# Kernel tuning notes

Measured on AMD Instinct MI355X. Metric: run time of the kernel, lower is better.

Reference implementation:

```python
import jax, jax.numpy as jnp
import numpy as np

EMBED = 512
HEADS = 8                      # num_heads
HD = EMBED // HEADS // 2       # diff-attn head dim = 32
EXP = 4
DEPTH = 1
LAMBDA_INIT = 0.8 - 0.6 * float(np.exp(-0.3 * (DEPTH - 1)))  # 0.2
EPS = 1e-5


def layernorm(x, w, b):
    mu = jnp.mean(x, axis=-1, keepdims=True)
    var = jnp.mean(jnp.square(x - mu), axis=-1, keepdims=True)
    return (x - mu) * jax.lax.rsqrt(var + EPS) * w + b


def rmsnorm(x, w):
    ms = jnp.mean(jnp.square(x), axis=-1, keepdims=True)
    return x * jax.lax.rsqrt(ms + EPS) * w


def setup_inputs() -> dict:
    key = jax.random.key(0)
    ks = jax.random.split(key, 12)
    B, N, D = 8, 1024, EMBED
    s = 0.02
    inp = {
        "x": jax.random.normal(ks[0], (B, N, D), jnp.float32),
        # diff-attention params
        "Wq": jax.random.normal(ks[1], (D, D), jnp.float32) * s,
        "Wk": jax.random.normal(ks[2], (D, D), jnp.float32) * s,
        "Wv": jax.random.normal(ks[3], (D, D), jnp.float32) * s,
        "Wo": jax.random.normal(ks[4], (D, D), jnp.float32) * s,
        "lq1": jax.random.normal(ks[5], (HD,), jnp.float32) * 0.1,
        "lk1": jax.random.normal(ks[6], (HD,), jnp.float32) * 0.1,
        "lq2": jax.random.normal(ks[7], (HD,), jnp.float32) * 0.1,
        "lk2": jax.random.normal(ks[8], (HD,), jnp.float32) * 0.1,
        "subln_w": jnp.ones((2 * HD,), jnp.float32),
        # block norms
        "n1_w": jnp.ones((D,), jnp.float32), "n1_b": jnp.zeros((D,), jnp.float32),
        "n2_w": jnp.ones((D,), jnp.float32), "n2_b": jnp.zeros((D,), jnp.float32),
        # MLP: LN(D) -> Linear(D,4D) -> GELU -> LN(4D) -> Linear(4D,D)
        "mln1_w": jnp.ones((D,), jnp.float32), "mln1_b": jnp.zeros((D,), jnp.float32),
        "mW1": jax.random.normal(ks[9], (EXP * D, D), jnp.float32) * s,
        "mb1": jnp.zeros((EXP * D,), jnp.float32),
        "mln2_w": jnp.ones((EXP * D,), jnp.float32), "mln2_b": jnp.zeros((EXP * D,), jnp.float32),
        "mW2": jax.random.normal(ks[10], (D, EXP * D), jnp.float32) * s,
        "mb2": jnp.zeros((D,), jnp.float32),
    }
    return inp


def diff_attn(x, Wq, Wk, Wv, Wo, lq1, lk1, lq2, lk2, subln_w):
    B, N, D = x.shape
    q = (x @ Wq.T).reshape(B, N, 2 * HEADS, HD).transpose(0, 2, 1, 3)   # [B,2H,N,hd]
    k = (x @ Wk.T).reshape(B, N, 2 * HEADS, HD).transpose(0, 2, 1, 3)   # [B,2H,N,hd]
    v = (x @ Wv.T).reshape(B, N, HEADS, 2 * HD).transpose(0, 2, 1, 3)   # [B,H,N,2hd]
    q = q * (HD ** -0.5)
    scores = jnp.einsum("bhnd,bhmd->bhnm", q, k)                        # [B,2H,N,N]
    attn = jax.nn.softmax(scores, axis=-1)
    attn = attn.reshape(B, HEADS, 2, N, N)
    lam1 = jnp.exp(jnp.sum(lq1 * lk1))
    lam2 = jnp.exp(jnp.sum(lq2 * lk2))
    lam = lam1 - lam2 + LAMBDA_INIT
    attn = attn[:, :, 0] - lam * attn[:, :, 1]                          # [B,H,N,N]
    out = jnp.einsum("bhnm,bhmd->bhnd", attn, v)                        # [B,H,N,2hd]
    out = rmsnorm(out, subln_w) * (1.0 - LAMBDA_INIT)
    out = out.transpose(0, 2, 1, 3).reshape(B, N, D)
    return out @ Wo.T


def reference(x, Wq, Wk, Wv, Wo, lq1, lk1, lq2, lk2, subln_w,
              n1_w, n1_b, n2_w, n2_b,
              mln1_w, mln1_b, mW1, mb1, mln2_w, mln2_b, mW2, mb2):
    x_res = x
    xn = layernorm(x, n1_w, n1_b)
    a = diff_attn(xn, Wq, Wk, Wv, Wo, lq1, lk1, lq2, lk2, subln_w)
    h = layernorm(a, n2_w, n2_b) + x_res
    # MLP
    z = layernorm(h, mln1_w, mln1_b)
    z = jax.nn.gelu(z @ mW1.T + mb1, approximate=False)
    z = layernorm(z, mln2_w, mln2_b)
    z = z @ mW2.T + mb2
    return z + h
```

## Files before the change

kernel.cpp:

```cpp
#include <hip/hip_runtime.h>
#include <cstdint>
#include <cstddef>

typedef unsigned short u16;
typedef unsigned int   u32;
typedef __attribute__((ext_vector_type(8))) short short8;
typedef __attribute__((ext_vector_type(4))) float floatx4;

__device__ __forceinline__ float asf(u32 u){ union{u32 u; float f;} v; v.u=u; return v.f; }
__device__ __forceinline__ u32 asu(float f){ union{float f; u32 u;} v; v.f=f; return v.u; }
__device__ __forceinline__ u16 f2bf(float f){ u32 u = asu(f); u32 r = u + 0x7FFFu + ((u>>16)&1u); return (u16)(r>>16); }
__device__ __forceinline__ u32 pack2(float a, float b){ return (u32)f2bf(a) | (((u32)f2bf(b))<<16); }
__device__ __forceinline__ void bf8f(uint4 d, float* o){
  o[0]=asf(d.x<<16); o[1]=asf(d.x&0xFFFF0000u);
  o[2]=asf(d.y<<16); o[3]=asf(d.y&0xFFFF0000u);
  o[4]=asf(d.z<<16); o[5]=asf(d.z&0xFFFF0000u);
  o[6]=asf(d.w<<16); o[7]=asf(d.w&0xFFFF0000u);
}

__global__ __launch_bounds__(256) void cvt_all(
    const float* __restrict__ Wq, const float* __restrict__ Wk,
    const float* __restrict__ Wv, const float* __restrict__ Wo,
    const float* __restrict__ W1, const float* __restrict__ W2,
    u16* __restrict__ Wqkv, u16* __restrict__ Wob,
    u16* __restrict__ W1b, u16* __restrict__ W2b)
{
  const int blk = blockIdx.x;
  const float* src; u16* dst; int off;
  if      (blk < 128)  { src = Wq; dst = Wqkv;          off = blk; }
  else if (blk < 256)  { src = Wk; dst = Wqkv + 262144; off = blk - 128; }
  else if (blk < 384)  { src = Wv; dst = Wqkv + 524288; off = blk - 256; }
  else if (blk < 512)  { src = Wo; dst = Wob;           off = blk - 384; }
  else if (blk < 1024) { src = W1; dst = W1b;           off = blk - 512; }
  else                 { src = W2; dst = W2b;           off = blk - 1024; }
  const int i = (off*256 + threadIdx.x)*8;
  const float4 a = *(const float4*)(src + i);
  const float4 b = *(const float4*)(src + i + 4);
  uint4 st;
  st.x = pack2(a.x, a.y); st.y = pack2(a.z, a.w);
  st.z = pack2(b.x, b.y); st.w = pack2(b.z, b.w);
  *(uint4*)(dst + i) = st;
}

enum { EPI_NONE=0, EPI_BIAS_GELU=1, EPI_BIAS_RES=2 };

template<int EPI, typename OutT>
__global__ __launch_bounds__(256) void gemm_bt(
    const u16* __restrict__ A, const u16* __restrict__ B,
    const float* __restrict__ bias, const float* __restrict__ res,
    OutT* __restrict__ C, int M, int N, int K)
{
  __shared__ u16 As[128*32];
  __shared__ u16 Bs[128*32];
  const int tid  = threadIdx.x;
  const int wave = tid >> 6;
  const int lane = tid & 63;
  const int bm = blockIdx.y, bn = blockIdx.x;

  const int srow = wave*16 + (lane>>2);
  const int scol = (lane&3)*8;
  const u16* Ag = A + (size_t)bm*128*K;
  const u16* Bg = B + (size_t)bn*128*K;

  const int wm = (wave>>1)*64;
  const int wn = (wave&1)*64;
  const int fr = lane & 15;
  const int fk = (lane>>4)*8;

  floatx4 acc[4][4] = {};

  for (int k0 = 0; k0 < K; k0 += 32) {
    __syncthreads();
    #pragma unroll
    for (int t = 0; t < 2; ++t) {
      __builtin_amdgcn_global_load_lds(
          (__attribute__((address_space(1))) void*)(Ag + (t*64 + srow)*K + k0 + scol),
          (__attribute__((address_space(3))) void*)(As + (t*64 + wave*16)*32),
          16, 0, 0);
      __builtin_amdgcn_global_load_lds(
          (__attribute__((address_space(1))) void*)(Bg + (t*64 + srow)*K + k0 + scol),
          (__attribute__((address_space(3))) void*)(Bs + (t*64 + wave*16)*32),
          16, 0, 0);
    }
    __syncthreads();

    short8 af[4], bfr[4];
    #pragma unroll
    for (int i=0;i<4;i++) af[i]  = *(const short8*)(As + (wm + i*16 + fr)*32 + fk);
    #pragma unroll
    for (int j=0;j<4;j++) bfr[j] = *(const short8*)(Bs + (wn + j*16 + fr)*32 + fk);
    #pragma unroll
    for (int i=0;i<4;i++)
      #pragma unroll
      for (int j=0;j<4;j++)
        acc[i][j] = __builtin_amdgcn_mfma_f32_16x16x32_bf16(af[i], bfr[j], acc[i][j], 0, 0, 0);
  }

  const int col0 = bn*128 + wn + fr;
  float bv[4] = {0.f,0.f,0.f,0.f};
  if constexpr (EPI != EPI_NONE) {
    #pragma unroll
    for (int j=0;j<4;j++) bv[j] = bias[col0 + j*16];
  }
  const int rq = (lane>>4)*4;
  #pragma unroll
  for (int i=0;i<4;i++){
    #pragma unroll
    for (int rr=0;rr<4;rr++){
      const int m = bm*128 + wm + i*16 + rq + rr;
      const size_t rowoff = (size_t)m*N;
      #pragma unroll
      for (int j=0;j<4;j++){
        float vv = acc[i][j][rr];
        const int n = col0 + j*16;
        if constexpr (EPI == EPI_BIAS_GELU){
          vv += bv[j];
          vv = 0.5f*vv*(1.f + erff(vv*0.70710678118654752f));
        } else if constexpr (EPI == EPI_BIAS_RES){
          vv += bv[j] + res[rowoff + n];
        }
        if constexpr (sizeof(OutT) == 2) C[rowoff + n] = f2bf(vv);
        else                             C[rowoff + n] = vv;
      }
    }
  }
}

__global__ __launch_bounds__(256) void ln512_kernel(
    const float* __restrict__ x, const float* __restrict__ w, const float* __restrict__ b,
    u16* __restrict__ out)
{
  const int row  = blockIdx.x*4 + (threadIdx.x>>6);
  const int lane = threadIdx.x & 63;
  const size_t base = (size_t)row*512 + lane*8;
  float v[8];
  { const float4 a = *(const float4*)(x + base);
    const float4 c = *(const float4*)(x + base + 4);
    v[0]=a.x; v[1]=a.y; v[2]=a.z; v[3]=a.w; v[4]=c.x; v[5]=c.y; v[6]=c.z; v[7]=c.w; }
  float s=0.f, sq=0.f;
  #pragma unroll
  for (int i=0;i<8;i++){ s += v[i]; sq += v[i]*v[i]; }
  for (int off=32; off>0; off>>=1){ s += __shfl_xor(s, off, 64); sq += __shfl_xor(sq, off, 64); }
  const float mu = s*(1.f/512.f);
  const float rs = rsqrtf(sq*(1.f/512.f) - mu*mu + 1e-5f);
  float o[8];
  #pragma unroll
  for (int i=0;i<8;i++)
    o[i] = (v[i]-mu)*rs*w[lane*8+i] + b[lane*8+i];
  uint4 st; st.x=pack2(o[0],o[1]); st.y=pack2(o[2],o[3]); st.z=pack2(o[4],o[5]); st.w=pack2(o[6],o[7]);
  *(uint4*)(out + base) = st;
}

__global__ __launch_bounds__(256) void lnres_kernel(
    const u16* __restrict__ ao, const float* __restrict__ x,
    const float* __restrict__ w2, const float* __restrict__ b2,
    const float* __restrict__ w3, const float* __restrict__ b3,
    float* __restrict__ h, u16* __restrict__ z)
{
  const int row  = blockIdx.x*4 + (threadIdx.x>>6);
  const int lane = threadIdx.x & 63;
  const size_t base = (size_t)row*512 + lane*8;
  float a[8], xr[8];
  bf8f(*(const uint4*)(ao + base), a);
  { const float4 p = *(const float4*)(x + base);
    const float4 q = *(const float4*)(x + base + 4);
    xr[0]=p.x; xr[1]=p.y; xr[2]=p.z; xr[3]=p.w; xr[4]=q.x; xr[5]=q.y; xr[6]=q.z; xr[7]=q.w; }
  float s=0.f, sq=0.f;
  #pragma unroll
  for (int i=0;i<8;i++){ s += a[i]; sq += a[i]*a[i]; }
  for (int off=32; off>0; off>>=1){ s += __shfl_xor(s, off, 64); sq += __shfl_xor(sq, off, 64); }
  float mu = s*(1.f/512.f);
  float rs = rsqrtf(sq*(1.f/512.f) - mu*mu + 1e-5f);
  float hv[8];
  #pragma unroll
  for (int i=0;i<8;i++)
    hv[i] = (a[i]-mu)*rs*w2[lane*8+i] + b2[lane*8+i] + xr[i];
  { float4 p; p.x=hv[0]; p.y=hv[1]; p.z=hv[2]; p.w=hv[3];
    float4 q; q.x=hv[4]; q.y=hv[5]; q.z=hv[6]; q.w=hv[7];
    *(float4*)(h + base) = p; *(float4*)(h + base + 4) = q; }
  s=0.f; sq=0.f;
  #pragma unroll
  for (int i=0;i<8;i++){ s += hv[i]; sq += hv[i]*hv[i]; }
  for (int off=32; off>0; off>>=1){ s += __shfl_xor(s, off, 64); sq += __shfl_xor(sq, off, 64); }
  mu = s*(1.f/512.f);
  rs = rsqrtf(sq*(1.f/512.f) - mu*mu + 1e-5f);
  float zv[8];
  #pragma unroll
  for (int i=0;i<8;i++)
    zv[i] = (hv[i]-mu)*rs*w3[lane*8+i] + b3[lane*8+i];
  uint4 st; st.x=pack2(zv[0],zv[1]); st.y=pack2(zv[2],zv[3]); st.z=pack2(zv[4],zv[5]); st.w=pack2(zv[6],zv[7]);
  *(uint4*)(z + base) = st;
}

__global__ __launch_bounds__(256) void ln2048_kernel(
    const u16* x, const float* __restrict__ w, const float* __restrict__ b,
    u16* out)
{
  const int row  = blockIdx.x*4 + (threadIdx.x>>6);
  const int lane = threadIdx.x & 63;
  const u16* xp = x + (size_t)row*2048;
  float v[32];
  #pragma unroll
  for (int g=0; g<4; ++g) bf8f(*(const uint4*)(xp + g*512 + lane*8), v + g*8);
  float s=0.f, sq=0.f;
  #pragma unroll
  for (int i=0;i<32;i++){ s += v[i]; sq += v[i]*v[i]; }
  for (int off=32; off>0; off>>=1){ s += __shfl_xor(s, off, 64); sq += __shfl_xor(sq, off, 64); }
  const float mu = s*(1.f/2048.f);
  const float rs = rsqrtf(sq*(1.f/2048.f) - mu*mu + 1e-5f);
  u16* op = out + (size_t)row*2048;
  #pragma unroll
  for (int g=0; g<4; ++g){
    float o[8];
    #pragma unroll
    for (int i=0;i<8;i++){
      const int idx = g*512 + lane*8 + i;
      o[i] = (v[g*8+i]-mu)*rs*w[idx] + b[idx];
    }
    uint4 st; st.x=pack2(o[0],o[1]); st.y=pack2(o[2],o[3]); st.z=pack2(o[4],o[5]); st.w=pack2(o[6],o[7]);
    *(uint4*)(op + g*512 + lane*8) = st;
  }
}

__global__ __launch_bounds__(256) void transpose_v(
    const u16* __restrict__ QKV, u16* __restrict__ Vt)
{
  __shared__ __align__(16) u16 T[64][72];
  const int bid = blockIdx.x;
  const int bh  = bid >> 4;
  const int kt  = bid & 15;
  const int b   = bh >> 3;
  const int h   = bh & 7;
  const int tid = threadIdx.x;

  const int key = tid >> 2;
  const int dc  = (tid & 3) * 16;
  const u16* src = QKV + ((size_t)(b*1024 + kt*64 + key))*1536 + 1024 + h*64 + dc;
  const uint4 a0 = *(const uint4*)(src);
  const uint4 a1 = *(const uint4*)(src + 8);
  *(uint4*)(&T[key][dc])     = a0;
  *(uint4*)(&T[key][dc + 8]) = a1;
  __syncthreads();

  const int d  = tid >> 2;
  const int kc = (tid & 3) * 16;
  union { uint4 q[2]; u16 us[16]; } ow;
  #pragma unroll
  for (int i=0;i<16;i++) ow.us[i] = T[kc + i][d];
  u16* dst = Vt + ((size_t)(bh*64 + d))*1024 + kt*64 + kc;
  *(uint4*)(dst)     = ow.q[0];
  *(uint4*)(dst + 8) = ow.q[1];
}

#define ATT_SCALE 0.17677669529663687f

__global__ __launch_bounds__(256) void attn_mfma(
    const u16* __restrict__ QKV, const u16* __restrict__ Vt,
    const float* __restrict__ lq1, const float* __restrict__ lk1,
    const float* __restrict__ lq2, const float* __restrict__ lk2,
    const float* __restrict__ subw, u16* __restrict__ out)
{
  __shared__ __align__(16) u16 Ks1[2][64*32];
  __shared__ __align__(16) u16 Ks2[2][64*32];
  __shared__ __align__(16) u16 Vs [2][64*64];
  __shared__ __align__(16) u16 Ps [2][4][16*32];

  const int tid  = threadIdx.x;
  const int wave = tid >> 6;
  const int lane = tid & 63;
  const int quad = lane >> 4;
  const int l15  = lane & 15;

  const int bid = blockIdx.x;
  const int bh  = bid >> 4;
  const int qt  = bid & 15;
  const int b   = bh >> 3;
  const int h   = bh & 7;

  float t1 = 0.f, t2 = 0.f;
  for (int i=0;i<32;i++){ t1 += lq1[i]*lk1[i]; t2 += lq2[i]*lk2[i]; }
  const float lam = __expf(t1) - __expf(t2) + 0.2f;

  const int qrowg = b*1024 + qt*64 + wave*16 + l15;
  const short8 aq1 = *(const short8*)(QKV + (size_t)qrowg*1536 + 2*h*32 + quad*8);
  const short8 aq2 = *(const short8*)(QKV + (size_t)qrowg*1536 + 2*h*32 + 32 + quad*8);

  floatx4 O1[4] = {}, O2[4] = {};
  float l1acc[4] = {0.f,0.f,0.f,0.f};
  float l2acc[4] = {0.f,0.f,0.f,0.f};
  const floatx4 zf4 = {0.f,0.f,0.f,0.f};

  const int kvbase = b*1024;
  u16* pw1 = &Ps[0][wave][0];
  u16* pw2 = &Ps[1][wave][0];

  const int kchunk = ((lane&3) ^ ((lane>>3)&3)) * 8;
  const u16* KbaseS = QKV + (size_t)(kvbase + wave*16 + (lane>>2))*1536 + 512 + 2*h*32 + kchunk;
  const int vchunk = ((lane&7) ^ (lane>>3)) * 8;
  const u16* VbaseS = Vt + ((size_t)bh*64 + wave*16 + (lane>>3))*1024 + vchunk;

  #define STAGE_TILE(buf, tt)                                                     \
    do {                                                                          \
      const u16* kp = KbaseS + (size_t)(tt)*64*1536;                              \
      __builtin_amdgcn_global_load_lds(                                           \
          (__attribute__((address_space(1))) void*)(kp),                          \
          (__attribute__((address_space(3))) void*)(&Ks1[buf][wave*16*32]), 16, 0, 0); \
      __builtin_amdgcn_global_load_lds(                                           \
          (__attribute__((address_space(1))) void*)(kp + 32),                     \
          (__attribute__((address_space(3))) void*)(&Ks2[buf][wave*16*32]), 16, 0, 0); \
      const u16* vp = VbaseS + (tt)*64;                                           \
      __builtin_amdgcn_global_load_lds(                                           \
          (__attribute__((address_space(1))) void*)(vp),                          \
          (__attribute__((address_space(3))) void*)(&Vs[buf][wave*16*64]), 16, 0, 0); \
      __builtin_amdgcn_global_load_lds(                                           \
          (__attribute__((address_space(1))) void*)(vp + (size_t)8*1024),         \
          (__attribute__((address_space(3))) void*)(&Vs[buf][(wave*16+8)*64]), 16, 0, 0); \
    } while (0)

  STAGE_TILE(0, 0);
  __syncthreads();

  const int kslotR = (quad ^ ((l15>>1)&3)) * 8;
  const int pslotR = ((quad + (l15>>2)) & 3) * 8;

  for (int t = 0; t < 16; ++t) {
    const int cur = t & 1;

    if (t < 15) STAGE_TILE(cur^1, t+1);

    #pragma unroll
    for (int kh = 0; kh < 2; ++kh) {
      #pragma unroll
      for (int ktl = 0; ktl < 2; ++ktl) {
        const int kt = kh*2 + ktl;
        const short8 bk1 = *(const short8*)(&Ks1[cur][(kt*16 + l15)*32 + kslotR]);
        const short8 bk2 = *(const short8*)(&Ks2[cur][(kt*16 + l15)*32 + kslotR]);
        const floatx4 s1 = __builtin_amdgcn_mfma_f32_16x16x32_bf16(aq1, bk1, zf4, 0, 0, 0);
        const floatx4 s2 = __builtin_amdgcn_mfma_f32_16x16x32_bf16(aq2, bk2, zf4, 0, 0, 0);
        const int wslot = ((ktl*2 + (l15>>3) + quad) & 3)*8;
        u16* d1 = pw1 + wslot + (l15&7);
        u16* d2 = pw2 + wslot + (l15&7);
        #pragma unroll
        for (int rr = 0; rr < 4; ++rr) {
          const float p1 = __expf(s1[rr]*ATT_SCALE);
          const float p2 = __expf(s2[rr]*ATT_SCALE);
          d1[(quad*4+rr)*32] = f2bf(p1);
          d2[(quad*4+rr)*32] = f2bf(p2);
          l1acc[rr] += p1;
          l2acc[rr] += p2;
        }
      }
      const short8 ap1 = *(const short8*)(pw1 + l15*32 + pslotR);
      const short8 ap2 = *(const short8*)(pw2 + l15*32 + pslotR);
      const int vslotR = ((kh*4 + quad) ^ (l15&7)) * 8;
      #pragma unroll
      for (int nt = 0; nt < 4; ++nt) {
        const short8 bv = *(const short8*)(&Vs[cur][(nt*16 + l15)*64 + vslotR]);
        O1[nt] = __builtin_amdgcn_mfma_f32_16x16x32_bf16(ap1, bv, O1[nt], 0, 0, 0);
        O2[nt] = __builtin_amdgcn_mfma_f32_16x16x32_bf16(ap2, bv, O2[nt], 0, 0, 0);
      }
    }

    if (t < 15) __syncthreads();
  }
  #undef STAGE_TILE

  #pragma unroll
  for (int rr=0; rr<4; ++rr){
    float v1 = l1acc[rr], v2 = l2acc[rr];
    v1 += __shfl_xor(v1, 1, 64); v2 += __shfl_xor(v2, 1, 64);
    v1 += __shfl_xor(v1, 2, 64); v2 += __shfl_xor(v2, 2, 64);
    v1 += __shfl_xor(v1, 4, 64); v2 += __shfl_xor(v2, 4, 64);
    v1 += __shfl_xor(v1, 8, 64); v2 += __shfl_xor(v2, 8, 64);
    l1acc[rr] = v1; l2acc[rr] = v2;
  }

  float sw[4];
  #pragma unroll
  for (int nt=0; nt<4; ++nt) sw[nt] = subw[nt*16 + l15];

  #pragma unroll
  for (int rr=0; rr<4; ++rr){
    const int row = quad*4 + rr;
    const float il1 = 1.f / l1acc[rr];
    const float cl2 = lam / l2acc[rr];
    float o[4]; float ss = 0.f;
    #pragma unroll
    for (int nt=0; nt<4; ++nt){
      o[nt] = O1[nt][rr]*il1 - O2[nt][rr]*cl2;
      ss += o[nt]*o[nt];
    }
    ss += __shfl_xor(ss, 1, 64);
    ss += __shfl_xor(ss, 2, 64);
    ss += __shfl_xor(ss, 4, 64);
    ss += __shfl_xor(ss, 8, 64);
    const float rs = rsqrtf(ss*(1.f/64.f) + 1e-5f) * 0.8f;
    const int orow = b*1024 + qt*64 + wave*16 + row;
    u16* op = out + (size_t)orow*512 + h*64 + l15;
    #pragma unroll
    for (int nt=0; nt<4; ++nt)
      op[nt*16] = f2bf(o[nt]*rs*sw[nt]);
  }
}

extern "C" void kernel_launch(void* const* d_in, const int* in_sizes, int n_in,
                              void* d_out, int out_size, void* d_ws, size_t ws_size,
                              hipStream_t stream)
{
  (void)in_sizes; (void)n_in; (void)out_size; (void)ws_size;
  const float* x    = (const float*)d_in[0];
  const float* Wq   = (const float*)d_in[1];
  const float* Wk   = (const float*)d_in[2];
  const float* Wv   = (const float*)d_in[3];
  const float* Wo   = (const float*)d_in[4];
  const float* lq1  = (const float*)d_in[5];
  const float* lk1  = (const float*)d_in[6];
  const float* lq2  = (const float*)d_in[7];
  const float* lk2  = (const float*)d_in[8];
  const float* subw = (const float*)d_in[9];
  const float* n1w  = (const float*)d_in[10];
  const float* n1b  = (const float*)d_in[11];
  const float* n2w  = (const float*)d_in[12];
  const float* n2b  = (const float*)d_in[13];
  const float* m1w  = (const float*)d_in[14];
  const float* m1b  = (const float*)d_in[15];
  const float* mW1  = (const float*)d_in[16];
  const float* mb1  = (const float*)d_in[17];
  const float* m2w  = (const float*)d_in[18];
  const float* m2b  = (const float*)d_in[19];
  const float* mW2  = (const float*)d_in[20];
  const float* mb2  = (const float*)d_in[21];
  float* out = (float*)d_out;

  char* ws = (char*)d_ws;
  const size_t MB = (size_t)1 << 20;
  u16*  xn  = (u16*)(ws + 0*MB);
  u16*  qkv = (u16*)(ws + 8*MB);
  u16*  a   = (u16*)(ws + 0*MB);
  u16*  ao  = (u16*)(ws + 8*MB);
  u16*  z1  = (u16*)(ws + 16*MB);
  float* h  = (float*)(ws + 32*MB);
  u16*  vt  = (u16*)(ws + 32*MB);
  u16*  t   = (u16*)(ws + 48*MB);
  u16* Wqkvb= (u16*)(ws + 80*MB);
  u16* Wob  = (u16*)(ws + 81*MB + 512*1024);
  u16* W1b  = (u16*)(ws + 82*MB);
  u16* W2b  = (u16*)(ws + 84*MB);

  const int M = 8192;

  cvt_all<<<1536, 256, 0, stream>>>(Wq, Wk, Wv, Wo, mW1, mW2, Wqkvb, Wob, W1b, W2b);

  ln512_kernel<<<2048, 256, 0, stream>>>(x, n1w, n1b, xn);

  gemm_bt<EPI_NONE,u16><<<dim3(12,64), 256, 0, stream>>>(xn, Wqkvb, nullptr, nullptr, qkv, M, 1536, 512);

  transpose_v<<<1024, 256, 0, stream>>>(qkv, vt);

  attn_mfma<<<1024, 256, 0, stream>>>(qkv, vt, lq1, lk1, lq2, lk2, subw, a);

  gemm_bt<EPI_NONE,u16><<<dim3(4,64), 256, 0, stream>>>(a, Wob, nullptr, nullptr, ao, M, 512, 512);

  lnres_kernel<<<2048, 256, 0, stream>>>(ao, x, n2w, n2b, m1w, m1b, h, z1);

  gemm_bt<EPI_BIAS_GELU,u16><<<dim3(16,64), 256, 0, stream>>>(z1, W1b, mb1, nullptr, t, M, 2048, 512);

  ln2048_kernel<<<2048, 256, 0, stream>>>(t, m2w, m2b, t);

  gemm_bt<EPI_BIAS_RES,float><<<dim3(4,64), 256, 0, stream>>>(t, W2b, mb2, h, out, M, 512, 2048);
}
```

Baseline: 336.1 us.

## Double-buffer GEMM LDS tiles and use cheaper bf16 rounding in attention

The GEMM main loop now keeps two LDS buffers for A and B. The global-to-LDS load of the next K slice is issued before the MFMAs on the current slice, which removes one barrier per iteration and overlaps load latency with compute. Separately, the attention P-matrix conversion to bf16 uses round-half-up instead of round-to-nearest-even, saving a few integer ops per element. The cost is double the GEMM LDS footprint, which may reduce occupancy, plus a slight change in rounding behaviour.

```diff
diff --git a/kernel.cpp b/kernel.cpp
--- a/kernel.cpp
+++ b/kernel.cpp
@@ -10,6 +10,7 @@
 __device__ __forceinline__ float asf(u32 u){ union{u32 u; float f;} v; v.u=u; return v.f; }
 __device__ __forceinline__ u32 asu(float f){ union{float f; u32 u;} v; v.f=f; return v.u; }
 __device__ __forceinline__ u16 f2bf(float f){ u32 u = asu(f); u32 r = u + 0x7FFFu + ((u>>16)&1u); return (u16)(r>>16); }
+__device__ __forceinline__ u16 f2bf_fast(float f){ return (u16)((asu(f) + 0x8000u)>>16); }
 __device__ __forceinline__ u32 pack2(float a, float b){ return (u32)f2bf(a) | (((u32)f2bf(b))<<16); }
 __device__ __forceinline__ void bf8f(uint4 d, float* o){
   o[0]=asf(d.x<<16); o[1]=asf(d.x&0xFFFF0000u);
@@ -50,8 +51,8 @@
     const float* __restrict__ bias, const float* __restrict__ res,
     OutT* __restrict__ C, int M, int N, int K)
 {
-  __shared__ u16 As[128*32];
-  __shared__ u16 Bs[128*32];
+  __shared__ u16 As[2][128*32];
+  __shared__ u16 Bs[2][128*32];
   const int tid  = threadIdx.x;
   const int wave = tid >> 6;
   const int lane = tid & 63;
@@ -69,32 +70,43 @@
 
   floatx4 acc[4][4] = {};
 
-  for (int k0 = 0; k0 < K; k0 += 32) {
-    __syncthreads();
-    #pragma unroll
-    for (int t = 0; t < 2; ++t) {
-      __builtin_amdgcn_global_load_lds(
-          (__attribute__((address_space(1))) void*)(Ag + (t*64 + srow)*K + k0 + scol),
-          (__attribute__((address_space(3))) void*)(As + (t*64 + wave*16)*32),
-          16, 0, 0);
-      __builtin_amdgcn_global_load_lds(
-          (__attribute__((address_space(1))) void*)(Bg + (t*64 + srow)*K + k0 + scol),
-          (__attribute__((address_space(3))) void*)(Bs + (t*64 + wave*16)*32),
-          16, 0, 0);
-    }
-    __syncthreads();
+  #define G_STAGE(buf, kk)                                                        \
+    do {                                                                          \
+      _Pragma("unroll")                                                           \
+      for (int tt = 0; tt < 2; ++tt) {                                            \
+        __builtin_amdgcn_global_load_lds(                                         \
+            (__attribute__((address_space(1))) void*)(Ag + (tt*64 + srow)*K + (kk) + scol), \
+            (__attribute__((address_space(3))) void*)(&As[buf][(tt*64 + wave*16)*32]),      \
+            16, 0, 0);                                                            \
+        __builtin_amdgcn_global_load_lds(                                         \
+            (__attribute__((address_space(1))) void*)(Bg + (tt*64 + srow)*K + (kk) + scol), \
+            (__attribute__((address_space(3))) void*)(&Bs[buf][(tt*64 + wave*16)*32]),      \
+            16, 0, 0);                                                            \
+      }                                                                           \
+    } while (0)
+
+  G_STAGE(0, 0);
+  __syncthreads();
+
+  const int nsteps = K >> 5;
+  for (int s = 0; s < nsteps; ++s) {
+    const int cur = s & 1;
+    if (s + 1 < nsteps) G_STAGE(cur^1, (s+1)*32);
 
     short8 af[4], bfr[4];
     #pragma unroll
-    for (int i=0;i<4;i++) af[i]  = *(const short8*)(As + (wm + i*16 + fr)*32 + fk);
-    #pragma unroll
-    for (int j=0;j<4;j++) bfr[j] = *(const short8*)(Bs + (wn + j*16 + fr)*32 + fk);
+    for (int i=0;i<4;i++) af[i]  = *(const short8*)(&As[cur][(wm + i*16 + fr)*32 + fk]);
+    #pragma unroll
+    for (int j=0;j<4;j++) bfr[j] = *(const short8*)(&Bs[cur][(wn + j*16 + fr)*32 + fk]);
     #pragma unroll
     for (int i=0;i<4;i++)
       #pragma unroll
       for (int j=0;j<4;j++)
         acc[i][j] = __builtin_amdgcn_mfma_f32_16x16x32_bf16(af[i], bfr[j], acc[i][j], 0, 0, 0);
-  }
+
+    if (s + 1 < nsteps) __syncthreads();
+  }
+  #undef G_STAGE
 
   const int col0 = bn*128 + wn + fr;
   float bv[4] = {0.f,0.f,0.f,0.f};
@@ -344,8 +356,8 @@
         for (int rr = 0; rr < 4; ++rr) {
           const float p1 = __expf(s1[rr]*ATT_SCALE);
           const float p2 = __expf(s2[rr]*ATT_SCALE);
-          d1[(quad*4+rr)*32] = f2bf(p1);
-          d2[(quad*4+rr)*32] = f2bf(p2);
+          d1[(quad*4+rr)*32] = f2bf_fast(p1);
+          d2[(quad*4+rr)*32] = f2bf_fast(p2);
           l1acc[rr] += p1;
           l2acc[rr] += p2;
         }
```

After: 323.0 us. -3.9%, faster.
